# Performance work log

Hardware: AMD Instinct MI355X
Metric: run time of the kernel (lower is better)

The kernel has to match this reference:

```python
import jax, jax.numpy as jnp
from jax import lax
import numpy as np

DEPTH = 6
DIM = 512            # embed_dim
DI = 768             # d_inner = int(1.5 * 512)
B = 64
IMG = 224
P = 16               # patch size == stride
HW = 14              # patches per side
NP = HW * HW         # 196


def _ln(x, w, b, eps=1e-5):
    m = jnp.mean(x, axis=-1, keepdims=True)
    v = jnp.var(x, axis=-1, keepdims=True)
    return (x - m) / jnp.sqrt(v + eps) * w + b


def _mamba(x, in_w, out_w, cw, cb, dw, db, A, D):
    # x: (N, L, DIM); in_w: (2*DI, DIM); out_w: (DIM, DI); cw: (DI, 3)
    xz = jnp.einsum('nlc,dc->nld', x, in_w)          # (N, L, 2*DI)
    xi, z = jnp.split(xz, 2, axis=-1)
    # depthwise conv1d, kernel=3, padding=1
    xp = jnp.pad(xi, ((0, 0), (1, 1), (0, 0)))
    xc = xp[:, :-2] * cw[:, 0] + xp[:, 1:-1] * cw[:, 1] + xp[:, 2:] * cw[:, 2] + cb
    xc = jax.nn.silu(xc)
    dt = jax.nn.softplus(jnp.einsum('nld,ed->nle', xc, dw) + db)
    Ae = jnp.exp(A * dt)                              # A < 0, dt > 0 -> stable
    y = jnp.cumsum(xc * dt * Ae, axis=1) * Ae + xc * D
    y = y * jax.nn.silu(z)
    return jnp.einsum('nld,cd->nlc', y, out_w)


def _forward(x, patch_w, patch_b, cls_token, pos_embed,
             blk_norm_w, blk_norm_b,
             mh_in_w, mh_out_w, mh_conv_w, mh_conv_b, mh_dt_w, mh_dt_b, mh_A, mh_D,
             mv_in_w, mv_out_w, mv_conv_w, mv_conv_b, mv_dt_w, mv_dt_b, mv_A, mv_D,
             fus_w, fus_b, ss_norm_w, ss_norm_b, fn_w, fn_b):
    Bsz = x.shape[0]
    # patch embed: Conv2d(3, DIM, k=16, s=16)
    feat = lax.conv_general_dilated(x, patch_w, window_strides=(P, P), padding='VALID',
                                    dimension_numbers=('NCHW', 'OIHW', 'NCHW'))
    feat = feat + patch_b[None, :, None, None]
    feat = feat.reshape(Bsz, DIM, NP).transpose(0, 2, 1)  # (B, 196, DIM)
    tok = jnp.concatenate([jnp.broadcast_to(cls_token, (Bsz, 1, DIM)), feat], axis=1)
    tok = tok + pos_embed                                  # (B, 197, DIM)
    for i in range(DEPTH):
        cls = tok[:, :1]
        pt = tok[:, 1:]
        pn = _ln(pt, blk_norm_w[i], blk_norm_b[i])
        p2 = pn.reshape(Bsz, HW, HW, DIM)
        # horizontal scan: rows as sequences
        yh = _mamba(p2.reshape(Bsz * HW, HW, DIM),
                    mh_in_w[i], mh_out_w[i], mh_conv_w[i], mh_conv_b[i],
                    mh_dt_w[i], mh_dt_b[i], mh_A[i], mh_D[i]).reshape(Bsz, HW, HW, DIM)
        # vertical scan: columns as sequences
        xv = p2.transpose(0, 2, 1, 3).reshape(Bsz * HW, HW, DIM)
        yv = _mamba(xv,
                    mv_in_w[i], mv_out_w[i], mv_conv_w[i], mv_conv_b[i],
                    mv_dt_w[i], mv_dt_b[i], mv_A[i], mv_D[i])
        yv = yv.reshape(Bsz, HW, HW, DIM).transpose(0, 2, 1, 3)
        yc = jnp.concatenate([yh, yv], axis=-1)            # (B, H, W, 2*DIM)
        yf = jnp.einsum('bhwk,ck->bhwc', yc, fus_w[i]) + fus_b[i]
        p_out = _ln(yf + p2, ss_norm_w[i], ss_norm_b[i]).reshape(Bsz, NP, DIM)
        cls_out = cls + _ln(cls, blk_norm_w[i], blk_norm_b[i])
        tok = jnp.concatenate([cls_out, p_out], axis=1)
    return _ln(tok, fn_w, fn_b)


def setup_inputs() -> dict:
    key = jax.random.key(0)
    ks = jax.random.split(key, 32)
    s = 0.02
    d = {}
    d['x'] = jax.random.normal(ks[0], (B, 3, IMG, IMG), jnp.float32)
    d['patch_w'] = jax.random.normal(ks[1], (DIM, 3, P, P), jnp.float32) * s
    d['patch_b'] = jnp.zeros((DIM,), jnp.float32)
    d['cls_token'] = jax.random.normal(ks[2], (1, 1, DIM), jnp.float32) * s
    d['pos_embed'] = jax.random.normal(ks[3], (1, NP + 1, DIM), jnp.float32) * s
    d['blk_norm_w'] = jnp.ones((DEPTH, DIM), jnp.float32)
    d['blk_norm_b'] = jnp.zeros((DEPTH, DIM), jnp.float32)
    for pfx, base in (('mh', 4), ('mv', 12)):
        d[pfx + '_in_w'] = jax.random.normal(ks[base + 0], (DEPTH, 2 * DI, DIM), jnp.float32) * s
        d[pfx + '_out_w'] = jax.random.normal(ks[base + 1], (DEPTH, DIM, DI), jnp.float32) * s
        d[pfx + '_conv_w'] = jax.random.normal(ks[base + 2], (DEPTH, DI, 3), jnp.float32) * 0.2
        d[pfx + '_conv_b'] = jnp.zeros((DEPTH, DI), jnp.float32)
        d[pfx + '_dt_w'] = jax.random.normal(ks[base + 3], (DEPTH, DI, DI), jnp.float32) * s
        d[pfx + '_dt_b'] = jnp.zeros((DEPTH, DI), jnp.float32)
        d[pfx + '_A'] = -jax.random.uniform(ks[base + 4], (DEPTH, DI), jnp.float32) * 0.1
        d[pfx + '_D'] = jnp.ones((DEPTH, DI), jnp.float32)
    d['fus_w'] = jax.random.normal(ks[20], (DEPTH, DIM, 2 * DIM), jnp.float32) * s
    d['fus_b'] = jnp.zeros((DEPTH, DIM), jnp.float32)
    d['ss_norm_w'] = jnp.ones((DEPTH, DIM), jnp.float32)
    d['ss_norm_b'] = jnp.zeros((DEPTH, DIM), jnp.float32)
    d['fn_w'] = jnp.ones((DIM,), jnp.float32)
    d['fn_b'] = jnp.zeros((DIM,), jnp.float32)
    return d


def reference(x, patch_w, patch_b, cls_token, pos_embed,
              blk_norm_w, blk_norm_b,
              mh_in_w, mh_out_w, mh_conv_w, mh_conv_b, mh_dt_w, mh_dt_b, mh_A, mh_D,
              mv_in_w, mv_out_w, mv_conv_w, mv_conv_b, mv_dt_w, mv_dt_b, mv_A, mv_D,
              fus_w, fus_b, ss_norm_w, ss_norm_b, fn_w, fn_b):
    return _forward(x, patch_w, patch_b, cls_token, pos_embed,
                    blk_norm_w, blk_norm_b,
                    mh_in_w, mh_out_w, mh_conv_w, mh_conv_b, mh_dt_w, mh_dt_b, mh_A, mh_D,
                    mv_in_w, mv_out_w, mv_conv_w, mv_conv_b, mv_dt_w, mv_dt_b, mv_A, mv_D,
                    fus_w, fus_b, ss_norm_w, ss_norm_b, fn_w, fn_b)
```

## Files before the change

### kernel.cpp

```cpp
#include <hip/hip_runtime.h>
#include <cstdint>


using u16 = unsigned short;
typedef __attribute__((ext_vector_type(8))) short   bfrag;
typedef __attribute__((ext_vector_type(4))) float   ffrag;
typedef __attribute__((ext_vector_type(8))) u16     u16x8;

__device__ __forceinline__ float b2f(u16 u) {
  union { float f; uint32_t i; } c; c.i = ((uint32_t)u) << 16; return c.f;
}
__device__ __forceinline__ u16 f2b(float f) {
  union { float f; uint32_t i; } c; c.f = f;
  uint32_t r = c.i + 0x7FFFu + ((c.i >> 16) & 1u);
  return (u16)(r >> 16);
}

#define LOG2E 1.44269504f
#define LN2   0.69314718f
__device__ __forceinline__ float fexp(float x) {
  return __builtin_amdgcn_exp2f(x * LOG2E);
}
__device__ __forceinline__ float fsigmoid(float x) {
  return __builtin_amdgcn_rcpf(1.f + __builtin_amdgcn_exp2f(-x * LOG2E));
}
__device__ __forceinline__ float fsilu(float x) { return x * fsigmoid(x); }
__device__ __forceinline__ float fsoftplus(float x) {
  float e = __builtin_amdgcn_exp2f(-fabsf(x) * LOG2E);
  return fmaxf(x, 0.f) + LN2 * __builtin_amdgcn_logf(1.f + e);
}

__device__ __forceinline__ void gl_lds16(const u16* g, u16* l) {
  __builtin_amdgcn_global_load_lds(
      (const __attribute__((address_space(1))) void*)g,
      (__attribute__((address_space(3))) void*)l,
      16, 0, 0);
}

__global__ __launch_bounds__(256, 2)
void gemm_dual(const u16* __restrict__ A, const u16* __restrict__ W1,
               const u16* __restrict__ W2, u16* __restrict__ C,
               int K, int lda, int ldc, int nsplit, int acol2, int ccol2)
{
  __shared__ u16 As[128 * 64];
  __shared__ u16 Bs[128 * 64];

  const int nb     = blockIdx.x;
  const bool second = nb >= nsplit;
  const u16* W     = second ? W2 : W1;
  const int n0l    = (nb - (second ? nsplit : 0)) * 128;
  const int acol   = second ? acol2 : 0;
  const int ccol0  = n0l + (second ? ccol2 : 0);
  const int m0     = blockIdx.y * 128;

  const int tid  = threadIdx.x;
  const int lane = tid & 63;
  const int wv   = tid >> 6;
  const int wm   = wv >> 1;
  const int wn   = wv & 1;

  const int lr   = lane >> 3;
  const int lc   = lane & 7;
  const int kcol = (lc ^ lr) << 3;

  const size_t abase = (size_t)(m0 + wv * 32 + lr) * lda + acol + kcol;
  const size_t wbase = (size_t)(n0l + wv * 32 + lr) * K + kcol;

  const ffrag fz = {0.f, 0.f, 0.f, 0.f};
  ffrag acc[4][4];
#pragma unroll
  for (int i = 0; i < 4; ++i)
#pragma unroll
    for (int j = 0; j < 4; ++j) acc[i][j] = fz;

  const int fr = lane & 15;
  const int fq = lane >> 4;

  for (int kb = 0; kb < K; kb += 64) {
#pragma unroll
    for (int i = 0; i < 4; ++i)
      gl_lds16(A + abase + (size_t)(i * 8) * lda + kb, &As[(wv * 4 + i) * 512]);
#pragma unroll
    for (int i = 0; i < 4; ++i)
      gl_lds16(W + wbase + (size_t)(i * 8) * K + kb, &Bs[(wv * 4 + i) * 512]);
    __syncthreads();

#pragma unroll
    for (int ks = 0; ks < 2; ++ks) {
      bfrag af[4], bfr[4];
#pragma unroll
      for (int t = 0; t < 4; ++t) {
        int r  = wm * 64 + t * 16 + fr;
        int ca = ((ks * 4 + fq) ^ (r & 7)) << 3;
        af[t]  = *(const bfrag*)&As[r * 64 + ca];
        int n  = wn * 64 + t * 16 + fr;
        int cb = ((ks * 4 + fq) ^ (n & 7)) << 3;
        bfr[t] = *(const bfrag*)&Bs[n * 64 + cb];
      }
#pragma unroll
      for (int i = 0; i < 4; ++i)
#pragma unroll
        for (int j = 0; j < 4; ++j)
          acc[i][j] = __builtin_amdgcn_mfma_f32_16x16x32_bf16(
              af[i], bfr[j], acc[i][j], 0, 0, 0);
    }
    __syncthreads();
  }

#pragma unroll
  for (int i = 0; i < 4; ++i) {
#pragma unroll
    for (int j = 0; j < 4; ++j) {
#pragma unroll
      for (int rg = 0; rg < 4; ++rg) {
        int row = m0 + wm * 64 + i * 16 + fq * 4 + rg;
        int col = ccol0 + wn * 64 + j * 16 + fr;
        C[(size_t)row * ldc + col] = f2b(acc[i][j][rg]);
      }
    }
  }
}

__global__ __launch_bounds__(256)
void k_cvt_all(const float* __restrict__ mhi, const float* __restrict__ mhd,
               const float* __restrict__ mho, const float* __restrict__ mvi,
               const float* __restrict__ mvd, const float* __restrict__ mvo,
               const float* __restrict__ fus, u16* __restrict__ dst)
{
  size_t e = ((size_t)blockIdx.x * 256 + threadIdx.x) * 8;
  int L = (int)(e / 4063232);
  int r = (int)(e - (size_t)L * 4063232);
  const float* s; int off;
  if      (r <  786432) { s = mhi + (size_t)L *  786432; off = r; }
  else if (r < 1376256) { s = mhd + (size_t)L *  589824; off = r -  786432; }
  else if (r < 1769472) { s = mho + (size_t)L *  393216; off = r - 1376256; }
  else if (r < 2555904) { s = mvi + (size_t)L *  786432; off = r - 1769472; }
  else if (r < 3145728) { s = mvd + (size_t)L *  589824; off = r - 2555904; }
  else if (r < 3538944) { s = mvo + (size_t)L *  393216; off = r - 3145728; }
  else                  { s = fus + (size_t)L *  524288; off = r - 3538944; }
  float4 a = *(const float4*)(s + off);
  float4 b = *(const float4*)(s + off + 4);
  u16x8 o;
  o[0] = f2b(a.x); o[1] = f2b(a.y); o[2] = f2b(a.z); o[3] = f2b(a.w);
  o[4] = f2b(b.x); o[5] = f2b(b.y); o[6] = f2b(b.z); o[7] = f2b(b.w);
  *(u16x8*)(dst + e) = o;
}

__global__ __launch_bounds__(256)
void k_cvt1(const float* __restrict__ s, u16* __restrict__ dst)
{
  int e = (blockIdx.x * 256 + threadIdx.x) * 8;
  float4 a = *(const float4*)(s + e);
  float4 b = *(const float4*)(s + e + 4);
  u16x8 o;
  o[0] = f2b(a.x); o[1] = f2b(a.y); o[2] = f2b(a.z); o[3] = f2b(a.w);
  o[4] = f2b(b.x); o[5] = f2b(b.y); o[6] = f2b(b.z); o[7] = f2b(b.w);
  *(u16x8*)(dst + e) = o;
}

__global__ __launch_bounds__(256) void k_im2col(const float* __restrict__ x,
                                                u16* __restrict__ im)
{
  int idx = blockIdx.x * 256 + threadIdx.x;
  int r = idx % 96, p = idx / 96;
  int b = p / 196, q = p - b * 196;
  int ph = q / 14, pw = q - ph * 14;
  int k = r * 8;
  int c = k >> 8, k2 = k & 255;
  int i = k2 >> 4, j = k2 & 15;
  const float* src = x + (((size_t)(b * 3 + c) * 224 + ph * 16 + i) * 224
                          + pw * 16 + j);
  float4 a = *(const float4*)src;
  float4 d = *(const float4*)(src + 4);
  u16x8 o;
  o[0] = f2b(a.x); o[1] = f2b(a.y); o[2] = f2b(a.z); o[3] = f2b(a.w);
  o[4] = f2b(d.x); o[5] = f2b(d.y); o[6] = f2b(d.z); o[7] = f2b(d.w);
  *(u16x8*)(im + (size_t)p * 768 + k) = o;
}

__global__ __launch_bounds__(256) void k_addbias(u16* __restrict__ TOK,
                                                 const float* __restrict__ pb,
                                                 const float* __restrict__ pos)
{
  int idx = blockIdx.x * 256 + threadIdx.x;
  int p = idx >> 6, n = (idx & 63) * 8;
  int tpos = 1 + (p % 196);
  u16x8 t = *(u16x8*)(TOK + (size_t)p * 512 + n);
  const float* pbv = pb + n;
  const float* pv  = pos + (size_t)tpos * 512 + n;
  u16x8 o;
#pragma unroll
  for (int i = 0; i < 8; ++i) o[i] = f2b(b2f(t[i]) + pbv[i] + pv[i]);
  *(u16x8*)(TOK + (size_t)p * 512 + n) = o;
}

__global__ __launch_bounds__(256) void k_ln(u16* __restrict__ T,
                                            const float* __restrict__ w,
                                            const float* __restrict__ b)
{
  int row  = blockIdx.x * 4 + (threadIdx.x >> 6);
  int lane = threadIdx.x & 63;
  int base = lane * 8;
  u16* p = T + (size_t)row * 512 + base;
  u16x8 t = *(u16x8*)p;
  float v[8]; float s = 0.f, qq = 0.f;
#pragma unroll
  for (int i = 0; i < 8; ++i) { v[i] = b2f(t[i]); s += v[i]; qq += v[i] * v[i]; }
#pragma unroll
  for (int o = 32; o; o >>= 1) { s += __shfl_xor(s, o, 64); qq += __shfl_xor(qq, o, 64); }
  float mean = s * (1.f / 512.f);
  float rstd = rsqrtf(qq * (1.f / 512.f) - mean * mean + 1e-5f);
  u16x8 ov;
#pragma unroll
  for (int i = 0; i < 8; ++i)
    ov[i] = f2b((v[i] - mean) * rstd * w[base + i] + b[base + i]);
  *(u16x8*)p = ov;
}

__global__ __launch_bounds__(256) void k_ln_fuse(const u16* __restrict__ YF,
                                                 u16* __restrict__ TOK,
                                                 const float* __restrict__ fb,
                                                 const float* __restrict__ w,
                                                 const float* __restrict__ b)
{
  int row  = blockIdx.x * 4 + (threadIdx.x >> 6);
  int lane = threadIdx.x & 63;
  int base = lane * 8;
  const u16* yf = YF + (size_t)row * 512 + base;
  u16* tp = TOK + (size_t)row * 512 + base;
  u16x8 yv = *(const u16x8*)yf;
  u16x8 tv = *(u16x8*)tp;
  float v[8]; float s = 0.f, qq = 0.f;
#pragma unroll
  for (int i = 0; i < 8; ++i) {
    v[i] = b2f(yv[i]) + fb[base + i] + b2f(tv[i]);
    s += v[i]; qq += v[i] * v[i];
  }
#pragma unroll
  for (int o = 32; o; o >>= 1) { s += __shfl_xor(s, o, 64); qq += __shfl_xor(qq, o, 64); }
  float mean = s * (1.f / 512.f);
  float rstd = rsqrtf(qq * (1.f / 512.f) - mean * mean + 1e-5f);
  u16x8 ov;
#pragma unroll
  for (int i = 0; i < 8; ++i)
    ov[i] = f2b((v[i] - mean) * rstd * w[base + i] + b[base + i]);
  *(u16x8*)tp = ov;
}

__global__ __launch_bounds__(256)
void k_conv_hv(const u16* __restrict__ XZ,
               const float* __restrict__ cwh, const float* __restrict__ cbh,
               const float* __restrict__ cwv, const float* __restrict__ cbv,
               u16* __restrict__ XC)
{
  int idx = blockIdx.x * 256 + threadIdx.x;
  int half = idx >= 688128;
  int t = idx - (half ? 688128 : 0);
  int d = t % 768, sq = t / 768;
  int rowbase, rowstride;
  if (!half) { rowbase = sq * 14; rowstride = 1; }
  else       { int b = sq / 14, wq = sq - b * 14; rowbase = b * 196 + wq; rowstride = 14; }
  const float* cw = half ? cwv : cwh;
  const float* cb = half ? cbv : cbh;
  int xio = half ? 1536 : 0, xco = half ? 768 : 0;
  float w0 = cw[d * 3 + 0], w1 = cw[d * 3 + 1], w2 = cw[d * 3 + 2];
  float bb = cb[d];
  float prev = 0.f, cur = b2f(XZ[(size_t)rowbase * 3072 + xio + d]), nxt;
#pragma unroll
  for (int l = 0; l < 14; ++l) {
    int row = rowbase + l * rowstride;
    nxt = (l < 13) ? b2f(XZ[(size_t)(row + rowstride) * 3072 + xio + d]) : 0.f;
    float u = prev * w0 + cur * w1 + nxt * w2 + bb;
    XC[(size_t)row * 1536 + xco + d] = f2b(fsilu(u));
    prev = cur; cur = nxt;
  }
}

__global__ __launch_bounds__(256)
void k_scan_hv(const u16* __restrict__ XZ, u16* __restrict__ XC,
               const float* __restrict__ dtbh, const float* __restrict__ Ah,
               const float* __restrict__ Dh,
               const float* __restrict__ dtbv, const float* __restrict__ Av,
               const float* __restrict__ Dv)
{
  int idx = blockIdx.x * 256 + threadIdx.x;
  int half = idx >= 688128;
  int t = idx - (half ? 688128 : 0);
  int d = t % 768, sq = t / 768;
  int rowbase, rowstride;
  if (!half) { rowbase = sq * 14; rowstride = 1; }
  else       { int b = sq / 14, wq = sq - b * 14; rowbase = b * 196 + wq; rowstride = 14; }
  int xio = half ? 1536 : 0, xco = half ? 768 : 0;
  float db = half ? dtbv[d] : dtbh[d];
  float Avv = half ? Av[d] : Ah[d];
  float Dvv = half ? Dv[d] : Dh[d];
  float run = 0.f;
#pragma unroll
  for (int l = 0; l < 14; ++l) {
    int row = rowbase + l * rowstride;
    size_t zb = (size_t)row * 3072 + xio;
    size_t cb = (size_t)row * 1536 + xco;
    float xc = b2f(XC[cb + d]);
    float dt = fsoftplus(b2f(XZ[zb + d]) + db);
    float ae = fexp(Avv * dt);
    run += xc * dt * ae;
    float z = b2f(XZ[zb + 768 + d]);
    float y = (run * ae + xc * Dvv) * (z * fsigmoid(z));
    XC[cb + d] = f2b(y);
  }
}

__global__ void k_cls(const float* __restrict__ cls_tok,
                      const float* __restrict__ pos,
                      const float* __restrict__ bw, const float* __restrict__ bb,
                      float* __restrict__ CLS)
{
  __shared__ float rs[8], rq[8], stat[2];
  int n = threadIdx.x;
  float v = cls_tok[n] + pos[n];
  for (int l = 0; l < 6; ++l) {
    float s = v, q = v * v;
#pragma unroll
    for (int o = 32; o; o >>= 1) { s += __shfl_xor(s, o, 64); q += __shfl_xor(q, o, 64); }
    if ((n & 63) == 0) { rs[n >> 6] = s; rq[n >> 6] = q; }
    __syncthreads();
    if (n == 0) {
      float S = 0.f, Q = 0.f;
      for (int i = 0; i < 8; ++i) { S += rs[i]; Q += rq[i]; }
      float m = S * (1.f / 512.f);
      stat[0] = m; stat[1] = rsqrtf(Q * (1.f / 512.f) - m * m + 1e-5f);
    }
    __syncthreads();
    float u = (v - stat[0]) * stat[1] * bw[l * 512 + n] + bb[l * 512 + n];
    v = v + u;
    __syncthreads();
  }
  CLS[n] = v;
}

__global__ __launch_bounds__(256) void k_final(const u16* __restrict__ TOK,
                                               const float* __restrict__ CLS,
                                               const float* __restrict__ w,
                                               const float* __restrict__ b,
                                               float* __restrict__ out)
{
  int row  = blockIdx.x * 4 + (threadIdx.x >> 6);
  int lane = threadIdx.x & 63;
  int bi = row / 197;
  int t  = row - bi * 197;
  int base = lane * 8;
  float v[8]; float s = 0.f, qq = 0.f;
  if (t == 0) {
#pragma unroll
    for (int i = 0; i < 8; ++i) v[i] = CLS[base + i];
  } else {
    const u16* src = TOK + ((size_t)bi * 196 + (t - 1)) * 512 + base;
    u16x8 tv = *(const u16x8*)src;
#pragma unroll
    for (int i = 0; i < 8; ++i) v[i] = b2f(tv[i]);
  }
#pragma unroll
  for (int i = 0; i < 8; ++i) { s += v[i]; qq += v[i] * v[i]; }
#pragma unroll
  for (int o = 32; o; o >>= 1) { s += __shfl_xor(s, o, 64); qq += __shfl_xor(qq, o, 64); }
  float mean = s * (1.f / 512.f);
  float rstd = rsqrtf(qq * (1.f / 512.f) - mean * mean + 1e-5f);
  float* op = out + (size_t)row * 512 + base;
#pragma unroll
  for (int i = 0; i < 8; ++i)
    op[i] = (v[i] - mean) * rstd * w[base + i] + b[base + i];
}

extern "C" void kernel_launch(void* const* d_in, const int* in_sizes, int n_in,
                              void* d_out, int out_size, void* d_ws, size_t ws_size,
                              hipStream_t stream)
{
  const float* x        = (const float*)d_in[0];
  const float* patch_w  = (const float*)d_in[1];
  const float* patch_b  = (const float*)d_in[2];
  const float* cls_tok  = (const float*)d_in[3];
  const float* pos      = (const float*)d_in[4];
  const float* blk_w    = (const float*)d_in[5];
  const float* blk_b    = (const float*)d_in[6];
  const float* mh_in_w  = (const float*)d_in[7];
  const float* mh_out_w = (const float*)d_in[8];
  const float* mh_cw    = (const float*)d_in[9];
  const float* mh_cb    = (const float*)d_in[10];
  const float* mh_dtw   = (const float*)d_in[11];
  const float* mh_dtb   = (const float*)d_in[12];
  const float* mh_A     = (const float*)d_in[13];
  const float* mh_D     = (const float*)d_in[14];
  const float* mv_in_w  = (const float*)d_in[15];
  const float* mv_out_w = (const float*)d_in[16];
  const float* mv_cw    = (const float*)d_in[17];
  const float* mv_cb    = (const float*)d_in[18];
  const float* mv_dtw   = (const float*)d_in[19];
  const float* mv_dtb   = (const float*)d_in[20];
  const float* mv_A     = (const float*)d_in[21];
  const float* mv_D     = (const float*)d_in[22];
  const float* fus_w    = (const float*)d_in[23];
  const float* fus_b    = (const float*)d_in[24];
  const float* ss_w     = (const float*)d_in[25];
  const float* ss_b     = (const float*)d_in[26];
  const float* fn_w     = (const float*)d_in[27];
  const float* fn_b     = (const float*)d_in[28];

  char* ws = (char*)d_ws;
  u16*   TOK  = (u16*)  (ws);
  u16*   XZHV = (u16*)  (ws +  12845056);
  u16*   XCHV = (u16*)  (ws +  89915392);
  u16*   YC   = (u16*)  (ws + 128450560);
  u16*   WB   = (u16*)  (ws + 154140672);
  u16*   WP   = (u16*)  (ws + 202899456);
  float* CLS  = (float*)(ws + 203685888);
  u16*   IM   = XCHV;
  u16*   YF   = XZHV;

  const size_t LS = 4063232;
  const size_t oMHI = 0,       oMHD = 786432,  oMHO = 1376256;
  const size_t oMVI = 1769472, oMVD = 2555904, oMVO = 3145728;
  const size_t oFUS = 3538944;

  k_cvt_all<<<11904, 256, 0, stream>>>(mh_in_w, mh_dtw, mh_out_w,
                                       mv_in_w, mv_dtw, mv_out_w, fus_w, WB);
  k_cvt1<<<192, 256, 0, stream>>>(patch_w, WP);
  k_im2col<<<4704, 256, 0, stream>>>(x, IM);
  gemm_dual<<<dim3(4, 98), 256, 0, stream>>>(IM, WP, WP, TOK,
                                             768, 768, 512, 4, 0, 0);
  k_addbias<<<3136, 256, 0, stream>>>(TOK, patch_b, pos);
  k_cls<<<1, 512, 0, stream>>>(cls_tok, pos, blk_w, blk_b, CLS);

  for (int L = 0; L < 6; ++L) {
    const u16* wl = WB + (size_t)L * LS;

    k_ln<<<3136, 256, 0, stream>>>(TOK, blk_w + L * 512, blk_b + L * 512);

    gemm_dual<<<dim3(24, 98), 256, 0, stream>>>(
        TOK, wl + oMHI, wl + oMVI, XZHV, 512, 512, 3072, 12, 0, 1536);
    k_conv_hv<<<5376, 256, 0, stream>>>(XZHV, mh_cw + L * 2304, mh_cb + L * 768,
                                        mv_cw + L * 2304, mv_cb + L * 768, XCHV);
    gemm_dual<<<dim3(12, 98), 256, 0, stream>>>(
        XCHV, wl + oMHD, wl + oMVD, XZHV, 768, 1536, 3072, 6, 768, 1536);
    k_scan_hv<<<5376, 256, 0, stream>>>(XZHV, XCHV,
                                        mh_dtb + L * 768, mh_A + L * 768, mh_D + L * 768,
                                        mv_dtb + L * 768, mv_A + L * 768, mv_D + L * 768);
    gemm_dual<<<dim3(8, 98), 256, 0, stream>>>(
        XCHV, wl + oMHO, wl + oMVO, YC, 768, 1536, 1024, 4, 768, 512);
    gemm_dual<<<dim3(4, 98), 256, 0, stream>>>(
        YC, wl + oFUS, wl + oFUS, YF, 1024, 1024, 512, 4, 0, 0);
    k_ln_fuse<<<3136, 256, 0, stream>>>(YF, TOK, fus_b + L * 512, ss_w + L * 512,
                                        ss_b + L * 512);
  }

  k_final<<<3152, 256, 0, stream>>>(TOK, CLS, fn_w, fn_b, (float*)d_out);
  (void)in_sizes; (void)n_in; (void)out_size; (void)ws_size;
}
```

Baseline: 1.496 ms.

## Fold out_proj into fusion weights, fuse LayerNorms, vectorize conv/scan, swizzle GEMM blocks

```diff
diff --git a/kernel.cpp b/kernel.cpp
--- a/kernel.cpp
+++ b/kernel.cpp
@@ -45,13 +45,19 @@
   __shared__ u16 As[128 * 64];
   __shared__ u16 Bs[128 * 64];
 
-  const int nb     = blockIdx.x;
-  const bool second = nb >= nsplit;
+  const int total = gridDim.x * gridDim.y;
+  const int flat  = blockIdx.y * gridDim.x + blockIdx.x;
+  const int chunk = total >> 3;
+  const int f2    = (flat & 7) * chunk + (flat >> 3);
+  const int bx    = f2 % gridDim.x;
+  const int by    = f2 / gridDim.x;
+
+  const bool second = bx >= nsplit;
   const u16* W     = second ? W2 : W1;
-  const int n0l    = (nb - (second ? nsplit : 0)) * 128;
+  const int n0l    = (bx - (second ? nsplit : 0)) * 128;
   const int acol   = second ? acol2 : 0;
   const int ccol0  = n0l + (second ? ccol2 : 0);
-  const int m0     = blockIdx.y * 128;
+  const int m0     = by * 128;
 
   const int tid  = threadIdx.x;
   const int lane = tid & 63;
@@ -108,17 +114,114 @@
   }
 
 #pragma unroll
-  for (int i = 0; i < 4; ++i) {
-#pragma unroll
-    for (int j = 0; j < 4; ++j) {
+  for (int i = 0; i < 4; ++i)
+#pragma unroll
+    for (int j = 0; j < 4; ++j)
 #pragma unroll
       for (int rg = 0; rg < 4; ++rg) {
         int row = m0 + wm * 64 + i * 16 + fq * 4 + rg;
         int col = ccol0 + wn * 64 + j * 16 + fr;
         C[(size_t)row * ldc + col] = f2b(acc[i][j][rg]);
       }
+}
+
+__global__ __launch_bounds__(256, 2)
+void gemm_wprep(const u16* __restrict__ WB, const u16* __restrict__ OT,
+                u16* __restrict__ WF)
+{
+  __shared__ u16 As[128 * 64];
+  __shared__ u16 Bs[128 * 64];
+
+  const int z = blockIdx.z, L = z >> 1, path = z & 1;
+  const u16* A = WB + (size_t)L * 4063232 + 3538944;
+  const u16* W = OT + (size_t)z * 393216;
+  u16* C = WF + (size_t)L * 786432;
+
+  const int m0 = blockIdx.y * 128, n0l = blockIdx.x * 128;
+  const int acol = path * 512, ccol = path * 768;
+
+  const int tid  = threadIdx.x;
+  const int lane = tid & 63;
+  const int wv   = tid >> 6;
+  const int wm   = wv >> 1;
+  const int wn   = wv & 1;
+  const int lr   = lane >> 3;
+  const int lc   = lane & 7;
+  const int kcol = (lc ^ lr) << 3;
+
+  const size_t abase = (size_t)(m0 + wv * 32 + lr) * 1024 + acol + kcol;
+  const size_t wbase = (size_t)(n0l + wv * 32 + lr) * 512 + kcol;
+
+  const ffrag fz = {0.f, 0.f, 0.f, 0.f};
+  ffrag acc[4][4];
+#pragma unroll
+  for (int i = 0; i < 4; ++i)
+#pragma unroll
+    for (int j = 0; j < 4; ++j) acc[i][j] = fz;
+
+  const int fr = lane & 15;
+  const int fq = lane >> 4;
+
+  for (int kb = 0; kb < 512; kb += 64) {
+#pragma unroll
+    for (int i = 0; i < 4; ++i)
+      gl_lds16(A + abase + (size_t)(i * 8) * 1024 + kb, &As[(wv * 4 + i) * 512]);
+#pragma unroll
+    for (int i = 0; i < 4; ++i)
+      gl_lds16(W + wbase + (size_t)(i * 8) * 512 + kb, &Bs[(wv * 4 + i) * 512]);
+    __syncthreads();
+
+#pragma unroll
+    for (int ks = 0; ks < 2; ++ks) {
+      bfrag af[4], bfr[4];
+#pragma unroll
+      for (int t = 0; t < 4; ++t) {
+        int r  = wm * 64 + t * 16 + fr;
+        int ca = ((ks * 4 + fq) ^ (r & 7)) << 3;
+        af[t]  = *(const bfrag*)&As[r * 64 + ca];
+        int n  = wn * 64 + t * 16 + fr;
+        int cb = ((ks * 4 + fq) ^ (n & 7)) << 3;
+        bfr[t] = *(const bfrag*)&Bs[n * 64 + cb];
+      }
+#pragma unroll
+      for (int i = 0; i < 4; ++i)
+#pragma unroll
+        for (int j = 0; j < 4; ++j)
+          acc[i][j] = __builtin_amdgcn_mfma_f32_16x16x32_bf16(
+              af[i], bfr[j], acc[i][j], 0, 0, 0);
     }
-  }
+    __syncthreads();
+  }
+
+#pragma unroll
+  for (int i = 0; i < 4; ++i)
+#pragma unroll
+    for (int j = 0; j < 4; ++j)
+#pragma unroll
+      for (int rg = 0; rg < 4; ++rg) {
+        int row = m0 + wm * 64 + i * 16 + fq * 4 + rg;
+        int col = ccol + n0l + wn * 64 + j * 16 + fr;
+        C[(size_t)row * 1536 + col] = f2b(acc[i][j][rg]);
+      }
+}
+
+__global__ __launch_bounds__(256)
+void k_transp(const float* __restrict__ mho, const float* __restrict__ mvo,
+              u16* __restrict__ OT)
+{
+  __shared__ float ld[32][33];
+  const int z = blockIdx.z, L = z >> 1, path = z & 1;
+  const float* src = (path ? mvo : mho) + (size_t)L * 393216;
+  u16* dst = OT + (size_t)z * 393216;
+  const int tx = threadIdx.x & 31, ty = threadIdx.x >> 5;
+  const int dx = blockIdx.x * 32, cy = blockIdx.y * 32;
+#pragma unroll
+  for (int i = 0; i < 4; ++i)
+    ld[ty + 8 * i][tx] = src[(size_t)(cy + ty + 8 * i) * 768 + dx + tx];
+  __syncthreads();
+#pragma unroll
+  for (int i = 0; i < 4; ++i)
+    dst[(size_t)(dx + ty + 8 * i) * 512 + cy + tx] = f2b(ld[tx][ty + 8 * i]);
 }
 
 __global__ __launch_bounds__(256)
@@ -178,34 +281,24 @@
   *(u16x8*)(im + (size_t)p * 768 + k) = o;
 }
 
-__global__ __launch_bounds__(256) void k_addbias(u16* __restrict__ TOK,
-                                                 const float* __restrict__ pb,
-                                                 const float* __restrict__ pos)
-{
-  int idx = blockIdx.x * 256 + threadIdx.x;
-  int p = idx >> 6, n = (idx & 63) * 8;
-  int tpos = 1 + (p % 196);
-  u16x8 t = *(u16x8*)(TOK + (size_t)p * 512 + n);
-  const float* pbv = pb + n;
-  const float* pv  = pos + (size_t)tpos * 512 + n;
-  u16x8 o;
-#pragma unroll
-  for (int i = 0; i < 8; ++i) o[i] = f2b(b2f(t[i]) + pbv[i] + pv[i]);
-  *(u16x8*)(TOK + (size_t)p * 512 + n) = o;
-}
-
-__global__ __launch_bounds__(256) void k_ln(u16* __restrict__ T,
-                                            const float* __restrict__ w,
-                                            const float* __restrict__ b)
+__global__ __launch_bounds__(256)
+void k_addbias_ln(u16* __restrict__ TOK, const float* __restrict__ pb,
+                  const float* __restrict__ pos, const float* __restrict__ w,
+                  const float* __restrict__ b)
 {
   int row  = blockIdx.x * 4 + (threadIdx.x >> 6);
   int lane = threadIdx.x & 63;
   int base = lane * 8;
-  u16* p = T + (size_t)row * 512 + base;
+  int tpos = 1 + (row % 196);
+  u16* p = TOK + (size_t)row * 512 + base;
   u16x8 t = *(u16x8*)p;
+  const float* pv = pos + (size_t)tpos * 512 + base;
   float v[8]; float s = 0.f, qq = 0.f;
 #pragma unroll
-  for (int i = 0; i < 8; ++i) { v[i] = b2f(t[i]); s += v[i]; qq += v[i] * v[i]; }
+  for (int i = 0; i < 8; ++i) {
+    v[i] = b2f(t[i]) + pb[base + i] + pv[i];
+    s += v[i]; qq += v[i] * v[i];
+  }
 #pragma unroll
   for (int o = 32; o; o >>= 1) { s += __shfl_xor(s, o, 64); qq += __shfl_xor(qq, o, 64); }
   float mean = s * (1.f / 512.f);
@@ -248,31 +341,81 @@
 }
 
 __global__ __launch_bounds__(256)
+void k_ln_fuse2(const u16* __restrict__ YF, u16* __restrict__ TOK,
+                const float* __restrict__ fb, const float* __restrict__ w1,
+                const float* __restrict__ b1, const float* __restrict__ w2,
+                const float* __restrict__ b2)
+{
+  int row  = blockIdx.x * 4 + (threadIdx.x >> 6);
+  int lane = threadIdx.x & 63;
+  int base = lane * 8;
+  const u16* yf = YF + (size_t)row * 512 + base;
+  u16* tp = TOK + (size_t)row * 512 + base;
+  u16x8 yv = *(const u16x8*)yf;
+  u16x8 tv = *(u16x8*)tp;
+  float v[8]; float s = 0.f, qq = 0.f;
+#pragma unroll
+  for (int i = 0; i < 8; ++i) {
+    v[i] = b2f(yv[i]) + fb[base + i] + b2f(tv[i]);
+    s += v[i]; qq += v[i] * v[i];
+  }
+#pragma unroll
+  for (int o = 32; o; o >>= 1) { s += __shfl_xor(s, o, 64); qq += __shfl_xor(qq, o, 64); }
+  float mean = s * (1.f / 512.f);
+  float rstd = rsqrtf(qq * (1.f / 512.f) - mean * mean + 1e-5f);
+  float s2 = 0.f, q2 = 0.f;
+#pragma unroll
+  for (int i = 0; i < 8; ++i) {
+    v[i] = (v[i] - mean) * rstd * w1[base + i] + b1[base + i];
+    s2 += v[i]; q2 += v[i] * v[i];
+  }
+#pragma unroll
+  for (int o = 32; o; o >>= 1) { s2 += __shfl_xor(s2, o, 64); q2 += __shfl_xor(q2, o, 64); }
+  float m2 = s2 * (1.f / 512.f);
+  float r2 = rsqrtf(q2 * (1.f / 512.f) - m2 * m2 + 1e-5f);
+  u16x8 ov;
+#pragma unroll
+  for (int i = 0; i < 8; ++i)
+    ov[i] = f2b((v[i] - m2) * r2 * w2[base + i] + b2[base + i]);
+  *(u16x8*)tp = ov;
+}
+
+__global__ __launch_bounds__(256)
 void k_conv_hv(const u16* __restrict__ XZ,
                const float* __restrict__ cwh, const float* __restrict__ cbh,
                const float* __restrict__ cwv, const float* __restrict__ cbv,
                u16* __restrict__ XC)
 {
   int idx = blockIdx.x * 256 + threadIdx.x;
-  int half = idx >= 688128;
-  int t = idx - (half ? 688128 : 0);
-  int d = t % 768, sq = t / 768;
+  int half = idx >= 344064;
+  int t = idx - (half ? 344064 : 0);
+  int dp = t % 384, sq = t / 384;
+  int d0 = dp * 2;
   int rowbase, rowstride;
   if (!half) { rowbase = sq * 14; rowstride = 1; }
   else       { int b = sq / 14, wq = sq - b * 14; rowbase = b * 196 + wq; rowstride = 14; }
   const float* cw = half ? cwv : cwh;
   const float* cb = half ? cbv : cbh;
   int xio = half ? 1536 : 0, xco = half ? 768 : 0;
-  float w0 = cw[d * 3 + 0], w1 = cw[d * 3 + 1], w2 = cw[d * 3 + 2];
-  float bb = cb[d];
-  float prev = 0.f, cur = b2f(XZ[(size_t)rowbase * 3072 + xio + d]), nxt;
+  float w0a = cw[d0 * 3 + 0], w1a = cw[d0 * 3 + 1], w2a = cw[d0 * 3 + 2];
+  float w0b = cw[d0 * 3 + 3], w1b = cw[d0 * 3 + 4], w2b = cw[d0 * 3 + 5];
+  float ba = cb[d0], bb = cb[d0 + 1];
+  uint32_t cu = *(const uint32_t*)&XZ[(size_t)rowbase * 3072 + xio + d0];
+  float pa = 0.f, pb = 0.f;
+  float ca = b2f((u16)cu), cbv2 = b2f((u16)(cu >> 16));
 #pragma unroll
   for (int l = 0; l < 14; ++l) {
     int row = rowbase + l * rowstride;
-    nxt = (l < 13) ? b2f(XZ[(size_t)(row + rowstride) * 3072 + xio + d]) : 0.f;
-    float u = prev * w0 + cur * w1 + nxt * w2 + bb;
-    XC[(size_t)row * 1536 + xco + d] = f2b(fsilu(u));
-    prev = cur; cur = nxt;
+    float na = 0.f, nb = 0.f;
+    if (l < 13) {
+      uint32_t nu = *(const uint32_t*)&XZ[(size_t)(row + rowstride) * 3072 + xio + d0];
+      na = b2f((u16)nu); nb = b2f((u16)(nu >> 16));
+    }
+    float ua = pa * w0a + ca * w1a + na * w2a + ba;
+    float ub = pb * w0b + cbv2 * w1b + nb * w2b + bb;
+    uint32_t ov = (uint32_t)f2b(fsilu(ua)) | ((uint32_t)f2b(fsilu(ub)) << 16);
+    *(uint32_t*)&XC[(size_t)row * 1536 + xco + d0] = ov;
+    pa = ca; pb = cbv2; ca = na; cbv2 = nb;
   }
 }
 
@@ -284,29 +427,39 @@
                const float* __restrict__ Dv)
 {
   int idx = blockIdx.x * 256 + threadIdx.x;
-  int half = idx >= 688128;
-  int t = idx - (half ? 688128 : 0);
-  int d = t % 768, sq = t / 768;
+  int half = idx >= 344064;
+  int t = idx - (half ? 344064 : 0);
+  int dp = t % 384, sq = t / 384;
+  int d0 = dp * 2;
   int rowbase, rowstride;
   if (!half) { rowbase = sq * 14; rowstride = 1; }
   else       { int b = sq / 14, wq = sq - b * 14; rowbase = b * 196 + wq; rowstride = 14; }
   int xio = half ? 1536 : 0, xco = half ? 768 : 0;
-  float db = half ? dtbv[d] : dtbh[d];
-  float Avv = half ? Av[d] : Ah[d];
-  float Dvv = half ? Dv[d] : Dh[d];
-  float run = 0.f;
+  const float* dtb = half ? dtbv : dtbh;
+  const float* Ap  = half ? Av : Ah;
+  const float* Dp  = half ? Dv : Dh;
+  float dba = dtb[d0], dbb = dtb[d0 + 1];
+  float Aa = Ap[d0], Ab = Ap[d0 + 1];
+  float Da = Dp[d0], Db = Dp[d0 + 1];
+  float ra = 0.f, rb = 0.f;
 #pragma unroll
   for (int l = 0; l < 14; ++l) {
     int row = rowbase + l * rowstride;
     size_t zb = (size_t)row * 3072 + xio;
-    size_t cb = (size_t)row * 1536 + xco;
-    float xc = b2f(XC[cb + d]);
-    float dt = fsoftplus(b2f(XZ[zb + d]) + db);
-    float ae = fexp(Avv * dt);
-    run += xc * dt * ae;
-    float z = b2f(XZ[zb + 768 + d]);
-    float y = (run * ae + xc * Dvv) * (z * fsigmoid(z));
-    XC[cb + d] = f2b(y);
+    size_t cbo = (size_t)row * 1536 + xco;
+    uint32_t xcu = *(const uint32_t*)&XC[cbo + d0];
+    uint32_t dtu = *(const uint32_t*)&XZ[zb + d0];
+    uint32_t zu  = *(const uint32_t*)&XZ[zb + 768 + d0];
+    float xca = b2f((u16)xcu), xcb = b2f((u16)(xcu >> 16));
+    float dta = fsoftplus(b2f((u16)dtu) + dba);
+    float dtbv2 = fsoftplus(b2f((u16)(dtu >> 16)) + dbb);
+    float aea = fexp(Aa * dta), aeb = fexp(Ab * dtbv2);
+    ra += xca * dta * aea;
+    rb += xcb * dtbv2 * aeb;
+    float za = b2f((u16)zu), zbv = b2f((u16)(zu >> 16));
+    float ya = (ra * aea + xca * Da) * (za * fsigmoid(za));
+    float yb = (rb * aeb + xcb * Db) * (zbv * fsigmoid(zbv));
+    *(uint32_t*)&XC[cbo + d0] = (uint32_t)f2b(ya) | ((uint32_t)f2b(yb) << 16);
   }
 }
 
@@ -409,47 +562,51 @@
   u16*   TOK  = (u16*)  (ws);
   u16*   XZHV = (u16*)  (ws +  12845056);
   u16*   XCHV = (u16*)  (ws +  89915392);
-  u16*   YC   = (u16*)  (ws + 128450560);
-  u16*   WB   = (u16*)  (ws + 154140672);
-  u16*   WP   = (u16*)  (ws + 202899456);
-  float* CLS  = (float*)(ws + 203685888);
+  u16*   WB   = (u16*)  (ws + 128450560);
+  u16*   WP   = (u16*)  (ws + 177209344);
+  u16*   OT   = (u16*)  (ws + 178782208);
+  u16*   WF   = (u16*)  (ws + 188219392);
+  float* CLS  = (float*)(ws + 197656576);
   u16*   IM   = XCHV;
   u16*   YF   = XZHV;
 
   const size_t LS = 4063232;
-  const size_t oMHI = 0,       oMHD = 786432,  oMHO = 1376256;
-  const size_t oMVI = 1769472, oMVD = 2555904, oMVO = 3145728;
-  const size_t oFUS = 3538944;
+  const size_t oMHI = 0, oMHD = 786432, oMVI = 1769472, oMVD = 2555904;
 
   k_cvt_all<<<11904, 256, 0, stream>>>(mh_in_w, mh_dtw, mh_out_w,
                                        mv_in_w, mv_dtw, mv_out_w, fus_w, WB);
+  k_transp<<<dim3(24, 16, 12), 256, 0, stream>>>(mh_out_w, mv_out_w, OT);
+  gemm_wprep<<<dim3(6, 4, 12), 256, 0, stream>>>(WB, OT, WF);
   k_cvt1<<<192, 256, 0, stream>>>(patch_w, WP);
   k_im2col<<<4704, 256, 0, stream>>>(x, IM);
   gemm_dual<<<dim3(4, 98), 256, 0, stream>>>(IM, WP, WP, TOK,
                                              768, 768, 512, 4, 0, 0);
-  k_addbias<<<3136, 256, 0, stream>>>(TOK, patch_b, pos);
+  k_addbias_ln<<<3136, 256, 0, stream>>>(TOK, patch_b, pos, blk_w, blk_b);
   k_cls<<<1, 512, 0, stream>>>(cls_tok, pos, blk_w, blk_b, CLS);
 
   for (int L = 0; L < 6; ++L) {
     const u16* wl = WB + (size_t)L * LS;
 
-    k_ln<<<3136, 256, 0, stream>>>(TOK, blk_w + L * 512, blk_b + L * 512);
-
     gemm_dual<<<dim3(24, 98), 256, 0, stream>>>(
         TOK, wl + oMHI, wl + oMVI, XZHV, 512, 512, 3072, 12, 0, 1536);
-    k_conv_hv<<<5376, 256, 0, stream>>>(XZHV, mh_cw + L * 2304, mh_cb + L * 768,
+    k_conv_hv<<<2688, 256, 0, stream>>>(XZHV, mh_cw + L * 2304, mh_cb + L * 768,
                                         mv_cw + L * 2304, mv_cb + L * 768, XCHV);
     gemm_dual<<<dim3(12, 98), 256, 0, stream>>>(
         XCHV, wl + oMHD, wl + oMVD, XZHV, 768, 1536, 3072, 6, 768, 1536);
-    k_scan_hv<<<5376, 256, 0, stream>>>(XZHV, XCHV,
+    k_scan_hv<<<2688, 256, 0, stream>>>(XZHV, XCHV,
                                         mh_dtb + L * 768, mh_A + L * 768, mh_D + L * 768,
                                         mv_dtb + L * 768, mv_A + L * 768, mv_D + L * 768);
-    gemm_dual<<<dim3(8, 98), 256, 0, stream>>>(
-        XCHV, wl + oMHO, wl + oMVO, YC, 768, 1536, 1024, 4, 768, 512);
     gemm_dual<<<dim3(4, 98), 256, 0, stream>>>(
-        YC, wl + oFUS, wl + oFUS, YF, 1024, 1024, 512, 4, 0, 0);
-    k_ln_fuse<<<3136, 256, 0, stream>>>(YF, TOK, fus_b + L * 512, ss_w + L * 512,
-                                        ss_b + L * 512);
+        XCHV, WF + (size_t)L * 786432, WF + (size_t)L * 786432, YF,
+        1536, 1536, 512, 4, 0, 0);
+    if (L < 5) {
+      k_ln_fuse2<<<3136, 256, 0, stream>>>(YF, TOK, fus_b + L * 512,
+                                           ss_w + L * 512, ss_b + L * 512,
+                                           blk_w + (L + 1) * 512, blk_b + (L + 1) * 512);
+    } else {
+      k_ln_fuse<<<3136, 256, 0, stream>>>(YF, TOK, fus_b + L * 512,
+                                          ss_w + L * 512, ss_b + L * 512);
+    }
   }
 
   k_final<<<3152, 256, 0, stream>>>(TOK, CLS, fn_w, fn_b, (float*)d_out);
```

Result: faster. 1.313 ms (-12.2%).
